# Kernel tuning notes

Measured on AMD Instinct MI355X. Metric: run time of the kernel, lower is better.

## Reference

```python
import jax, jax.numpy as jnp
import numpy as np
import math

N_HEAD = 16

def setup_inputs() -> dict:
    key = jax.random.key(0)
    k1, k2, k3, k4, k5 = jax.random.split(key, 5)
    B, S, D = 2, 2048, 1024
    return {
        "hidden_states": jax.random.normal(k1, (B, S, D), dtype=jnp.float32),
        "c_attn_w": jax.random.normal(k2, (D, 3 * D), dtype=jnp.float32) * 0.02,
        "c_attn_b": jax.random.normal(k3, (3 * D,), dtype=jnp.float32) * 0.02,
        "c_proj_w": jax.random.normal(k4, (D, D), dtype=jnp.float32) * 0.02,
        "c_proj_b": jax.random.normal(k5, (D,), dtype=jnp.float32) * 0.02,
    }

def reference(hidden_states, c_attn_w, c_attn_b, c_proj_w, c_proj_b):
    B, S, D = hidden_states.shape
    H = N_HEAD
    hd = D // H
    # GPT-2 Conv1D: x @ W + b, W is [in, out]
    qkv = hidden_states @ c_attn_w + c_attn_b            # [B,S,3D]
    q, k, v = jnp.split(qkv, 3, axis=-1)                 # each [B,S,D]
    # sparsify_q/k/v_fn are identity hooks in this config
    def to_heads(x):
        return x.reshape(B, S, H, hd).transpose(0, 2, 1, 3)  # [B,H,S,hd]
    q, k, v = to_heads(q), to_heads(k), to_heads(v)
    scores = jnp.einsum("bhqd,bhkd->bhqk", q, k) / math.sqrt(hd)  # [B,H,S,S]
    causal = jnp.triu(jnp.ones((S, S), dtype=bool), k=1)
    scores = jnp.where(causal, jnp.finfo(scores.dtype).min, scores)
    attn = jax.nn.softmax(scores, axis=-1)
    out = jnp.einsum("bhqk,bhkd->bhqd", attn, v)         # [B,H,S,hd]
    out = out.transpose(0, 2, 1, 3).reshape(B, S, D)
    return out @ c_proj_w + c_proj_b
```

## Files before the change

kernel.cpp:

```cpp
#include <hip/hip_runtime.h>
#include <stdint.h>


#define B_   2
#define S_   2048
#define D_   1024
#define H_   16
#define HD_  64

typedef __bf16 bf16x8 __attribute__((ext_vector_type(8)));
typedef float  f32x4  __attribute__((ext_vector_type(4)));
typedef float  f32x16 __attribute__((ext_vector_type(16)));
typedef uint32_t u32x4 __attribute__((ext_vector_type(4)));

__device__ __forceinline__ float b2f(uint16_t u) {
    union { uint32_t i; float f; } x; x.i = ((uint32_t)u) << 16; return x.f;
}
__device__ __forceinline__ uint16_t f2b(float f) {
    uint32_t x = __builtin_bit_cast(uint32_t, f);
    x += 0x7fffu + ((x >> 16) & 1u);
    return (uint16_t)(x >> 16);
}
__device__ __forceinline__ float sq(float f) {
    return fminf(fmaxf(f, -1e4f), 1e4f);
}
__device__ __forceinline__ void async16(const void* g, void* l) {
    __builtin_amdgcn_global_load_lds(
        (const __attribute__((address_space(1))) void*)g,
        (__attribute__((address_space(3))) void*)l, 16, 0, 0);
}

__global__ __launch_bounds__(64)
void kcode(uint16_t* out, float v) { if (threadIdx.x == 0) out[0] = f2b(v); }

__device__ __forceinline__ void cvt4(const float* __restrict__ in,
                                     uint16_t* __restrict__ out, int i) {
    float4 v = *(const float4*)(in + i);
    ushort4 o;
    o.x = f2b(v.x); o.y = f2b(v.y); o.z = f2b(v.z); o.w = f2b(v.w);
    *(ushort4*)(out + i) = o;
}

__device__ __forceinline__ void trans_body(const float* __restrict__ in,
                                           uint16_t* __restrict__ out,
                                           int rows, int cols, int bxx, int byy,
                                           int tid, uint16_t (*tile)[68]) {
    const int tx = tid & 15, ty = tid >> 4;
    const int c0 = bxx * 64, r0 = byy * 64;
#pragma unroll
    for (int p = 0; p < 4; ++p) {
        int rr = ty + p * 16;
        float4 v = *(const float4*)(in + (size_t)(r0 + rr) * cols + c0 + tx * 4);
        tile[rr][tx * 4 + 0] = f2b(v.x);
        tile[rr][tx * 4 + 1] = f2b(v.y);
        tile[rr][tx * 4 + 2] = f2b(v.z);
        tile[rr][tx * 4 + 3] = f2b(v.w);
    }
    __syncthreads();
#pragma unroll
    for (int p = 0; p < 4; ++p) {
        int rr = ty + p * 16;
        ushort4 v;
        v.x = tile[tx * 4 + 0][rr];
        v.y = tile[tx * 4 + 1][rr];
        v.z = tile[tx * 4 + 2][rr];
        v.w = tile[tx * 4 + 3][rr];
        *(ushort4*)(out + (size_t)(c0 + rr) * rows + r0 + tx * 4) = v;
    }
}

__global__ __launch_bounds__(256)
void kprep(const float* __restrict__ hid, const float* __restrict__ ab,
           const float* __restrict__ pb, const float* __restrict__ wA,
           const float* __restrict__ wP, uint16_t* __restrict__ HO,
           uint16_t* __restrict__ bA, uint16_t* __restrict__ bP,
           uint16_t* __restrict__ WtA, uint16_t* __restrict__ WtP) {
    __shared__ __attribute__((aligned(16))) uint16_t tile[64][68];
    const int bx = (int)blockIdx.x, tid = threadIdx.x;
    if (bx < 4096) {
        cvt4(hid, HO, (bx * 256 + tid) * 4);
    } else if (bx < 4100) {
        int i = ((bx - 4096) * 256 + tid) * 4;
        const float* src = (i < 3072) ? ab + i : pb + (i - 3072);
        uint16_t*   dst = (i < 3072) ? bA + i : bP + (i - 3072);
        float4 v = *(const float4*)src;
        ushort4 o;
        o.x = f2b(v.x); o.y = f2b(v.y); o.z = f2b(v.z); o.w = f2b(v.w);
        *(ushort4*)dst = o;
    } else if (bx < 4868) {
        int bb = bx - 4100;
        trans_body(wA, WtA, 1024, 3072, bb % 48, bb / 48, tid, tile);
    } else {
        int bb = bx - 4868;
        trans_body(wP, WtP, 1024, 1024, bb % 16, bb / 16, tid, tile);
    }
}

__global__ __launch_bounds__(256, 2)
void kgemm_qkv(const uint16_t* __restrict__ A, const uint16_t* __restrict__ Bt,
               const uint16_t* __restrict__ bias,
               uint16_t* __restrict__ Qb, uint16_t* __restrict__ Kb,
               uint16_t* __restrict__ Vt) {
    constexpr int KD = 1024;
    __shared__ __attribute__((aligned(16))) uint16_t smem[2][8192];
    const int tid = threadIdx.x, lane = tid & 63, wid = tid >> 6;
    const int r = lane & 15, qd = lane >> 4;
    const int bm = blockIdx.x * 128, bn = blockIdx.y * 128;
    const int wm = (wid & 1) * 64, wn = (wid >> 1) * 64;
    const int sel = (int)blockIdx.y >> 3;
    f32x4 acc[4][4] = {};

    auto stage = [&](int k0, int buf) {
        uint16_t* As = smem[buf];
        uint16_t* Bs = smem[buf] + 4096;
#pragma unroll
        for (int half = 0; half < 2; ++half) {
            int s = half * 256 + tid;
            int row = s >> 2;
            int kq = (s & 3) ^ (row & 3);
            async16(A  + (size_t)(bm + row) * KD + k0 + kq * 8, As + s * 8);
            async16(Bt + (size_t)(bn + row) * KD + k0 + kq * 8, Bs + s * 8);
        }
    };

    stage(0, 0);

    if (sel != 2) {
        for (int t = 0; t < 32; ++t) {
            __syncthreads();
            if (t + 1 < 32) stage((t + 1) * 32, (t + 1) & 1);
            const uint16_t* As = smem[t & 1];
            const uint16_t* Bs = smem[t & 1] + 4096;
            bf16x8 af[4], bfr[4];
#pragma unroll
            for (int i = 0; i < 4; ++i) {
                int ra = wm + i * 16 + r;
                af[i]  = *(const bf16x8*)(As + ((ra * 4) + (qd ^ (ra & 3))) * 8);
                int rb = wn + i * 16 + r;
                bfr[i] = *(const bf16x8*)(Bs + ((rb * 4) + (qd ^ (rb & 3))) * 8);
            }
#pragma unroll
            for (int i = 0; i < 4; ++i)
#pragma unroll
                for (int j = 0; j < 4; ++j)
                    acc[i][j] = __builtin_amdgcn_mfma_f32_16x16x32_bf16(
                        bfr[j], af[i], acc[i][j], 0, 0, 0);
        }
        const float SCq = 0.1803368801111204f;
        uint16_t* dst = sel ? Kb : Qb;
#pragma unroll
        for (int j = 0; j < 4; ++j) {
            int n0 = bn + wn + j * 16 + qd * 4;
            ushort4 b4 = *(const ushort4*)(bias + n0);
            float bv0 = b2f(b4.x), bv1 = b2f(b4.y),
                  bv2 = b2f(b4.z), bv3 = b2f(b4.w);
            int d = n0 & 1023, h = d >> 6, e0 = d & 63;
#pragma unroll
            for (int i = 0; i < 4; ++i) {
                int m = bm + wm + i * 16 + r;
                int bb = m >> 11, s = m & 2047;
                float v0 = acc[i][j][0] + bv0, v1 = acc[i][j][1] + bv1,
                      v2 = acc[i][j][2] + bv2, v3 = acc[i][j][3] + bv3;
                if (sel == 0) { v0 *= SCq; v1 *= SCq; v2 *= SCq; v3 *= SCq; }
                ushort4 o;
                o.x = f2b(sq(v0)); o.y = f2b(sq(v1));
                o.z = f2b(sq(v2)); o.w = f2b(sq(v3));
                *(ushort4*)(dst + (((size_t)bb * H_ + h) * S_ + s) * HD_ + e0) = o;
            }
        }
    } else {
        for (int t = 0; t < 32; ++t) {
            __syncthreads();
            if (t + 1 < 32) stage((t + 1) * 32, (t + 1) & 1);
            const uint16_t* As = smem[t & 1];
            const uint16_t* Bs = smem[t & 1] + 4096;
            bf16x8 af[4], bfr[4];
#pragma unroll
            for (int i = 0; i < 4; ++i) {
                int ra = wm + i * 16 + r;
                af[i]  = *(const bf16x8*)(As + ((ra * 4) + (qd ^ (ra & 3))) * 8);
                int rb = wn + i * 16 + r;
                bfr[i] = *(const bf16x8*)(Bs + ((rb * 4) + (qd ^ (rb & 3))) * 8);
            }
#pragma unroll
            for (int i = 0; i < 4; ++i)
#pragma unroll
                for (int j = 0; j < 4; ++j)
                    acc[i][j] = __builtin_amdgcn_mfma_f32_16x16x32_bf16(
                        af[i], bfr[j], acc[i][j], 0, 0, 0);
        }
#pragma unroll
        for (int j = 0; j < 4; ++j) {
            int n = bn + wn + j * 16 + r;
            float bv = b2f(bias[n]);
            int d = n & 1023, h = d >> 6, e = d & 63;
#pragma unroll
            for (int i = 0; i < 4; ++i) {
                int m0 = bm + wm + i * 16 + qd * 4;
                int bb = m0 >> 11, s0 = m0 & 2047;
                ushort4 o;
                o.x = f2b(sq(acc[i][j][0] + bv));
                o.y = f2b(sq(acc[i][j][1] + bv));
                o.z = f2b(sq(acc[i][j][2] + bv));
                o.w = f2b(sq(acc[i][j][3] + bv));
                *(ushort4*)(Vt + (((size_t)bb * H_ + h) * HD_ + e) * S_ + s0) = o;
            }
        }
    }
}

__global__ __launch_bounds__(256, 2)
void kgemm_proj(const uint16_t* __restrict__ A, const uint16_t* __restrict__ Bt,
                const uint16_t* __restrict__ bias, float* __restrict__ out) {
    constexpr int KD = 1024;
    __shared__ __attribute__((aligned(16))) uint16_t smem[2][6144];
    const int tid = threadIdx.x, lane = tid & 63, wid = tid >> 6;
    const int r = lane & 15, qd = lane >> 4;
    const int bm = blockIdx.x * 64, bn = blockIdx.y * 128;
    const int wm = (wid & 1) * 32, wn = (wid >> 1) * 64;
    f32x4 acc[2][4] = {};

    auto stage = [&](int k0, int buf) {
        uint16_t* As = smem[buf];
        uint16_t* Bs = smem[buf] + 2048;
        {
            int s = tid;
            int row = s >> 2;
            int kq = (s & 3) ^ (row & 3);
            async16(A + (size_t)(bm + row) * KD + k0 + kq * 8, As + s * 8);
        }
#pragma unroll
        for (int half = 0; half < 2; ++half) {
            int s = half * 256 + tid;
            int row = s >> 2;
            int kq = (s & 3) ^ (row & 3);
            async16(Bt + (size_t)(bn + row) * KD + k0 + kq * 8, Bs + s * 8);
        }
    };

    stage(0, 0);

    for (int t = 0; t < 32; ++t) {
        __syncthreads();
        if (t + 1 < 32) stage((t + 1) * 32, (t + 1) & 1);
        const uint16_t* As = smem[t & 1];
        const uint16_t* Bs = smem[t & 1] + 2048;
        bf16x8 af[2], bfr[4];
#pragma unroll
        for (int i = 0; i < 2; ++i) {
            int ra = wm + i * 16 + r;
            af[i] = *(const bf16x8*)(As + ((ra * 4) + (qd ^ (ra & 3))) * 8);
        }
#pragma unroll
        for (int j = 0; j < 4; ++j) {
            int rb = wn + j * 16 + r;
            bfr[j] = *(const bf16x8*)(Bs + ((rb * 4) + (qd ^ (rb & 3))) * 8);
        }
#pragma unroll
        for (int i = 0; i < 2; ++i)
#pragma unroll
            for (int j = 0; j < 4; ++j)
                acc[i][j] = __builtin_amdgcn_mfma_f32_16x16x32_bf16(
                    bfr[j], af[i], acc[i][j], 0, 0, 0);
    }

#pragma unroll
    for (int i = 0; i < 2; ++i) {
        int m = bm + wm + i * 16 + r;
#pragma unroll
        for (int j = 0; j < 4; ++j) {
            int n0 = bn + wn + j * 16 + qd * 4;
            ushort4 b4 = *(const ushort4*)(bias + n0);
            float4 o;
            o.x = sq(acc[i][j][0] + b2f(b4.x));
            o.y = sq(acc[i][j][1] + b2f(b4.y));
            o.z = sq(acc[i][j][2] + b2f(b4.z));
            o.w = sq(acc[i][j][3] + b2f(b4.w));
            *(float4*)(out + (size_t)m * 1024 + n0) = o;
        }
    }
}

__global__ __launch_bounds__(256, 4)
void kattn(const uint16_t* __restrict__ Q, const uint16_t* __restrict__ K,
           const uint16_t* __restrict__ Vt, uint16_t* __restrict__ O) {
    const int d_  = (int)blockIdx.y * 32 + (int)blockIdx.x;
    const int bh  = (d_ & 7) + 8 * ((d_ >> 3) & 3);
    const int qt  = 31 - (d_ >> 5);
    const int tid = threadIdx.x, lane = tid & 63, wid = tid >> 6;
    const int c = lane & 31, hh = lane >> 5;
    const int wq = wid >> 1, wk = wid & 1;
    const uint16_t* Qb = Q  + (size_t)bh * S_ * HD_;
    const int b = bh >> 4, h = bh & 15;

    __shared__ __attribute__((aligned(16))) uint16_t smem[4][4096];
    __shared__ float lsx[4][64];

    const int T = qt + 1;

    const int sA = tid, sB = 256 + tid;
    const int krA = sA >> 3, kcA = (sA & 7) ^ (krA & 7);
    const int krB = sB >> 3, kcB = (sB & 7) ^ (krB & 7);
    const uint16_t* ksA = K  + (size_t)bh * S_ * HD_ + (size_t)krA * HD_ + kcA * 8;
    const uint16_t* ksB = K  + (size_t)bh * S_ * HD_ + (size_t)krB * HD_ + kcB * 8;
    const uint16_t* vsA = Vt + (size_t)bh * HD_ * S_ + (size_t)krA * S_ + kcA * 8;
    const uint16_t* vsB = Vt + (size_t)bh * HD_ * S_ + (size_t)krB * S_ + kcB * 8;

    auto stageto = [&](int buf) {
        async16(ksA, &smem[buf][sA * 8]);
        async16(ksB, &smem[buf][sB * 8]);
        async16(vsA, &smem[2 + buf][sA * 8]);
        async16(vsB, &smem[2 + buf][sB * 8]);
        ksA += 64 * HD_; ksB += 64 * HD_;
        vsA += 64;       vsB += 64;
    };

    stageto(0);

    const int q0 = qt * 64;
    const int qg = q0 + wq * 32 + c;
    bf16x8 qf[4];
#pragma unroll
    for (int cc = 0; cc < 4; ++cc)
        qf[cc] = *(const bf16x8*)(Qb + (size_t)qg * HD_ + cc * 16 + hh * 8);

    const int krow = wk * 32 + c;
    const int kofs0 = krow * 64 + (((0 + hh) ^ (krow & 7)) * 8);
    const int kofs1 = krow * 64 + (((2 + hh) ^ (krow & 7)) * 8);
    const int kofs2 = krow * 64 + (((4 + hh) ^ (krow & 7)) * 8);
    const int kofs3 = krow * 64 + (((6 + hh) ^ (krow & 7)) * 8);
    const int vgA = ((4 * wk + 0 + hh) ^ (c & 7)) * 8;
    const int vgB = ((4 * wk + 2 + hh) ^ (c & 7)) * 8;
    const int vofs00 = c * 64 + vgA,        vofs01 = c * 64 + vgB;
    const int vofs10 = (32 + c) * 64 + vgA, vofs11 = (32 + c) * 64 + vgB;

    const f32x16 ZERO = {};
    f32x16 oacc0 = {}, oacc1 = {};
    float lsum = 0.f;

    auto iter = [&](int buf, int t, bool pf) {
        __syncthreads();
        if (pf) stageto(buf ^ 1);

        const uint16_t* Kc = smem[buf];
        const uint16_t* Vc = smem[2 + buf];

        __builtin_amdgcn_s_setprio(1);
        bf16x8 kf0 = *(const bf16x8*)(Kc + kofs0);
        bf16x8 kf1 = *(const bf16x8*)(Kc + kofs1);
        bf16x8 kf2 = *(const bf16x8*)(Kc + kofs2);
        bf16x8 kf3 = *(const bf16x8*)(Kc + kofs3);
        f32x16 sacc;
        sacc = __builtin_amdgcn_mfma_f32_32x32x16_bf16(kf0, qf[0], ZERO, 0, 0, 0);
        sacc = __builtin_amdgcn_mfma_f32_32x32x16_bf16(kf1, qf[1], sacc, 0, 0, 0);
        sacc = __builtin_amdgcn_mfma_f32_32x32x16_bf16(kf2, qf[2], sacc, 0, 0, 0);
        sacc = __builtin_amdgcn_mfma_f32_32x32x16_bf16(kf3, qf[3], sacc, 0, 0, 0);
        __builtin_amdgcn_s_setprio(0);

        if (t == T - 1) {
            const int kvb = t * 64 + wk * 32 + 4 * hh;
#pragma unroll
            for (int r = 0; r < 16; ++r) {
                int kvgl = kvb + (r & 3) + 8 * (r >> 2);
                if (kvgl > qg) sacc[r] = -3e38f;
            }
        }

        float p[16];
#pragma unroll
        for (int r = 0; r < 16; ++r)
            p[r] = exp2f(fminf(sacc[r], 20.f));
#pragma unroll
        for (int r = 0; r < 16; r += 4)
            lsum += ((p[r] + p[r + 1]) + (p[r + 2] + p[r + 3]));

        uint32_t D[8];
#pragma unroll
        for (int m = 0; m < 8; ++m)
            asm("v_cvt_pk_bf16_f32 %0, %1, %2"
                : "=v"(D[m]) : "v"(p[2 * m]), "v"(p[2 * m + 1]));
        asm("v_permlane32_swap_b32 %0, %1" : "+v"(D[0]), "+v"(D[2]));
        asm("v_permlane32_swap_b32 %0, %1" : "+v"(D[1]), "+v"(D[3]));
        asm("v_permlane32_swap_b32 %0, %1" : "+v"(D[4]), "+v"(D[6]));
        asm("v_permlane32_swap_b32 %0, %1" : "+v"(D[5]), "+v"(D[7]));
        u32x4 w0, w1;
        w0[0] = D[0]; w0[1] = D[1]; w0[2] = D[2]; w0[3] = D[3];
        w1[0] = D[4]; w1[1] = D[5]; w1[2] = D[6]; w1[3] = D[7];
        bf16x8 pf0 = __builtin_bit_cast(bf16x8, w0);
        bf16x8 pf1 = __builtin_bit_cast(bf16x8, w1);

        __builtin_amdgcn_s_setprio(1);
        bf16x8 v00 = *(const bf16x8*)(Vc + vofs00);
        bf16x8 v10 = *(const bf16x8*)(Vc + vofs01);
        bf16x8 v01 = *(const bf16x8*)(Vc + vofs10);
        bf16x8 v11 = *(const bf16x8*)(Vc + vofs11);
        oacc0 = __builtin_amdgcn_mfma_f32_32x32x16_bf16(pf0, v00, oacc0, 0, 0, 0);
        oacc0 = __builtin_amdgcn_mfma_f32_32x32x16_bf16(pf1, v10, oacc0, 0, 0, 0);
        oacc1 = __builtin_amdgcn_mfma_f32_32x32x16_bf16(pf0, v01, oacc1, 0, 0, 0);
        oacc1 = __builtin_amdgcn_mfma_f32_32x32x16_bf16(pf1, v11, oacc1, 0, 0, 0);
        __builtin_amdgcn_s_setprio(0);
    };

    int t = 0;
    while (t + 2 <= T) {
        iter(0, t, true);
        iter(1, t + 1, t + 2 < T);
        t += 2;
    }
    if (t < T) iter(0, t, false);

    lsum += __shfl_xor(lsum, 32);
    __syncthreads();
    float* xch = (float*)&smem[0][0];
    float* myA = xch + wid * 2048;
#pragma unroll
    for (int s = 0; s < 4; ++s) {
        f32x4 a0, a1;
#pragma unroll
        for (int g = 0; g < 4; ++g) { a0[g] = oacc0[4 * s + g]; a1[g] = oacc1[4 * s + g]; }
        *(f32x4*)(myA + 0 * 1024 + s * 256 + lane * 4) = a0;
        *(f32x4*)(myA + 1 * 1024 + s * 256 + lane * 4) = a1;
    }
    lsx[wid][lane] = lsum;
    __syncthreads();
    const int pwid = wid ^ 1;
    float lfull = lsum + lsx[pwid][lane];
    float osum[16];
#pragma unroll
    for (int s = 0; s < 4; ++s) {
        f32x4 po = *(const f32x4*)(xch + pwid * 2048 + wk * 1024 + s * 256 + lane * 4);
#pragma unroll
        for (int g = 0; g < 4; ++g)
            osum[4 * s + g] = (wk ? oacc1[4 * s + g] : oacc0[4 * s + g]) + po[g];
    }
#pragma unroll
    for (int r = 0; r < 16; ++r) {
        int qp = (r & 3) + 8 * (r >> 2) + 4 * hh;
        float inv = 1.0f / __shfl(lfull, qp);
        int qglob = q0 + wq * 32 + qp;
        int hd = wk * 32 + c;
        O[((size_t)b * S_ + qglob) * D_ + h * HD_ + hd] = f2b(sq(osum[r] * inv));
    }
}

extern "C" void kernel_launch(void* const* d_in, const int* in_sizes, int n_in,
                              void* d_out, int out_size, void* d_ws, size_t ws_size,
                              hipStream_t stream) {
    uint16_t* ws = (uint16_t*)d_ws;

    const int exp_sizes[5] = {4194304, 3145728, 3072, 1048576, 1024};
    if (n_in != 5) { kcode<<<1, 64, 0, stream>>>((uint16_t*)d_out, 2950.f); return; }
    for (int i = 0; i < 5; ++i)
        if (in_sizes[i] != exp_sizes[i]) {
            kcode<<<1, 64, 0, stream>>>((uint16_t*)d_out, 3000.f + 100.f * i); return;
        }
    if (out_size != 4194304) { kcode<<<1, 64, 0, stream>>>((uint16_t*)d_out, 2900.f); return; }

    uint16_t* WtA = ws;
    uint16_t* WtP = WtA + 3145728;
    uint16_t* bA  = WtP + 1048576;
    uint16_t* bP  = bA  + 4096;
    uint16_t* Qb  = bP  + 4096;
    uint16_t* Kb  = Qb  + 4194304;
    uint16_t* Vt  = Kb  + 4194304;
    uint16_t* HO  = Vt  + 4194304;
    const size_t NEED = (size_t)((HO + 4194304) - ws) * 2 + 16;
    if (ws_size < NEED) {
        kcode<<<1, 64, 0, stream>>>((uint16_t*)d_out, 1000.f + (float)(ws_size >> 20));
        return;
    }

    kprep<<<5124, 256, 0, stream>>>((const float*)d_in[0], (const float*)d_in[2],
                                    (const float*)d_in[4], (const float*)d_in[1],
                                    (const float*)d_in[3], HO, bA, bP, WtA, WtP);

    kgemm_qkv<<<dim3(32, 24), 256, 0, stream>>>(HO, WtA, bA, Qb, Kb, Vt);
    kattn<<<dim3(32, 32), 256, 0, stream>>>(Qb, Kb, Vt, HO);
    kgemm_proj<<<dim3(64, 8), 256, 0, stream>>>(HO, WtP, bP, (float*)d_out);
}
```

Before: 174.9 us.

## Double GEMM K-step per stage and triple-buffer attention with 128-row query tiles

Both GEMM kernels now stage 64 K-columns per barrier instead of 32. This halves the number of syncthreads and doubles the shared-memory buffers. The attention kernel moves to 512-thread blocks covering 128 query rows, with a three-deep K/V ring buffer that uses explicit vmcnt waits instead of full syncthreads. The output reduction is split into two passes to fit the smaller exchange buffer. These changes aim to cut barrier overhead and improve load/compute overlap, at the cost of more LDS per block, which may lower occupancy, and more complex causal-tail handling.

After: 325.7 us. +86.2%, slower.

```diff
diff --git a/kernel.cpp b/kernel.cpp
--- a/kernel.cpp
+++ b/kernel.cpp
@@ -102,7 +102,7 @@
                uint16_t* __restrict__ Qb, uint16_t* __restrict__ Kb,
                uint16_t* __restrict__ Vt) {
     constexpr int KD = 1024;
-    __shared__ __attribute__((aligned(16))) uint16_t smem[2][8192];
+    __shared__ __attribute__((aligned(16))) uint16_t smem[2][16384];
     const int tid = threadIdx.x, lane = tid & 63, wid = tid >> 6;
     const int r = lane & 15, qd = lane >> 4;
     const int bm = blockIdx.x * 128, bn = blockIdx.y * 128;
@@ -112,39 +112,46 @@
 
     auto stage = [&](int k0, int buf) {
         uint16_t* As = smem[buf];
-        uint16_t* Bs = smem[buf] + 4096;
-#pragma unroll
-        for (int half = 0; half < 2; ++half) {
-            int s = half * 256 + tid;
-            int row = s >> 2;
-            int kq = (s & 3) ^ (row & 3);
-            async16(A  + (size_t)(bm + row) * KD + k0 + kq * 8, As + s * 8);
-            async16(Bt + (size_t)(bn + row) * KD + k0 + kq * 8, Bs + s * 8);
-        }
+        uint16_t* Bs = smem[buf] + 8192;
+#pragma unroll
+        for (int hh = 0; hh < 2; ++hh)
+#pragma unroll
+            for (int half = 0; half < 2; ++half) {
+                int s = half * 256 + tid;
+                int row = s >> 2;
+                int kq = (s & 3) ^ (row & 3);
+                async16(A  + (size_t)(bm + row) * KD + k0 + hh * 32 + kq * 8,
+                        As + hh * 4096 + s * 8);
+                async16(Bt + (size_t)(bn + row) * KD + k0 + hh * 32 + kq * 8,
+                        Bs + hh * 4096 + s * 8);
+            }
     };
 
     stage(0, 0);
 
     if (sel != 2) {
-        for (int t = 0; t < 32; ++t) {
+        for (int t = 0; t < 16; ++t) {
             __syncthreads();
-            if (t + 1 < 32) stage((t + 1) * 32, (t + 1) & 1);
-            const uint16_t* As = smem[t & 1];
-            const uint16_t* Bs = smem[t & 1] + 4096;
-            bf16x8 af[4], bfr[4];
-#pragma unroll
-            for (int i = 0; i < 4; ++i) {
-                int ra = wm + i * 16 + r;
-                af[i]  = *(const bf16x8*)(As + ((ra * 4) + (qd ^ (ra & 3))) * 8);
-                int rb = wn + i * 16 + r;
-                bfr[i] = *(const bf16x8*)(Bs + ((rb * 4) + (qd ^ (rb & 3))) * 8);
-            }
-#pragma unroll
-            for (int i = 0; i < 4; ++i)
-#pragma unroll
-                for (int j = 0; j < 4; ++j)
-                    acc[i][j] = __builtin_amdgcn_mfma_f32_16x16x32_bf16(
-                        bfr[j], af[i], acc[i][j], 0, 0, 0);
+            if (t + 1 < 16) stage((t + 1) * 64, (t + 1) & 1);
+#pragma unroll
+            for (int hh = 0; hh < 2; ++hh) {
+                const uint16_t* As = smem[t & 1] + hh * 4096;
+                const uint16_t* Bs = smem[t & 1] + 8192 + hh * 4096;
+                bf16x8 af[4], bfr[4];
+#pragma unroll
+                for (int i = 0; i < 4; ++i) {
+                    int ra = wm + i * 16 + r;
+                    af[i]  = *(const bf16x8*)(As + ((ra * 4) + (qd ^ (ra & 3))) * 8);
+                    int rb = wn + i * 16 + r;
+                    bfr[i] = *(const bf16x8*)(Bs + ((rb * 4) + (qd ^ (rb & 3))) * 8);
+                }
+#pragma unroll
+                for (int i = 0; i < 4; ++i)
+#pragma unroll
+                    for (int j = 0; j < 4; ++j)
+                        acc[i][j] = __builtin_amdgcn_mfma_f32_16x16x32_bf16(
+                            bfr[j], af[i], acc[i][j], 0, 0, 0);
+            }
         }
         const float SCq = 0.1803368801111204f;
         uint16_t* dst = sel ? Kb : Qb;
@@ -169,25 +176,28 @@
             }
         }
     } else {
-        for (int t = 0; t < 32; ++t) {
+        for (int t = 0; t < 16; ++t) {
             __syncthreads();
-            if (t + 1 < 32) stage((t + 1) * 32, (t + 1) & 1);
-            const uint16_t* As = smem[t & 1];
-            const uint16_t* Bs = smem[t & 1] + 4096;
-            bf16x8 af[4], bfr[4];
-#pragma unroll
-            for (int i = 0; i < 4; ++i) {
-                int ra = wm + i * 16 + r;
-                af[i]  = *(const bf16x8*)(As + ((ra * 4) + (qd ^ (ra & 3))) * 8);
-                int rb = wn + i * 16 + r;
-                bfr[i] = *(const bf16x8*)(Bs + ((rb * 4) + (qd ^ (rb & 3))) * 8);
-            }
-#pragma unroll
-            for (int i = 0; i < 4; ++i)
-#pragma unroll
-                for (int j = 0; j < 4; ++j)
-                    acc[i][j] = __builtin_amdgcn_mfma_f32_16x16x32_bf16(
-                        af[i], bfr[j], acc[i][j], 0, 0, 0);
+            if (t + 1 < 16) stage((t + 1) * 64, (t + 1) & 1);
+#pragma unroll
+            for (int hh = 0; hh < 2; ++hh) {
+                const uint16_t* As = smem[t & 1] + hh * 4096;
+                const uint16_t* Bs = smem[t & 1] + 8192 + hh * 4096;
+                bf16x8 af[4], bfr[4];
+#pragma unroll
+                for (int i = 0; i < 4; ++i) {
+                    int ra = wm + i * 16 + r;
+                    af[i]  = *(const bf16x8*)(As + ((ra * 4) + (qd ^ (ra & 3))) * 8);
+                    int rb = wn + i * 16 + r;
+                    bfr[i] = *(const bf16x8*)(Bs + ((rb * 4) + (qd ^ (rb & 3))) * 8);
+                }
+#pragma unroll
+                for (int i = 0; i < 4; ++i)
+#pragma unroll
+                    for (int j = 0; j < 4; ++j)
+                        acc[i][j] = __builtin_amdgcn_mfma_f32_16x16x32_bf16(
+                            af[i], bfr[j], acc[i][j], 0, 0, 0);
+            }
         }
 #pragma unroll
         for (int j = 0; j < 4; ++j) {
@@ -213,7 +223,7 @@
 void kgemm_proj(const uint16_t* __restrict__ A, const uint16_t* __restrict__ Bt,
                 const uint16_t* __restrict__ bias, float* __restrict__ out) {
     constexpr int KD = 1024;
-    __shared__ __attribute__((aligned(16))) uint16_t smem[2][6144];
+    __shared__ __attribute__((aligned(16))) uint16_t smem[2][12288];
     const int tid = threadIdx.x, lane = tid & 63, wid = tid >> 6;
     const int r = lane & 15, qd = lane >> 4;
     const int bm = blockIdx.x * 64, bn = blockIdx.y * 128;
@@ -222,46 +232,54 @@
 
     auto stage = [&](int k0, int buf) {
         uint16_t* As = smem[buf];
-        uint16_t* Bs = smem[buf] + 2048;
-        {
-            int s = tid;
-            int row = s >> 2;
-            int kq = (s & 3) ^ (row & 3);
-            async16(A + (size_t)(bm + row) * KD + k0 + kq * 8, As + s * 8);
-        }
-#pragma unroll
-        for (int half = 0; half < 2; ++half) {
-            int s = half * 256 + tid;
-            int row = s >> 2;
-            int kq = (s & 3) ^ (row & 3);
-            async16(Bt + (size_t)(bn + row) * KD + k0 + kq * 8, Bs + s * 8);
+        uint16_t* Bs = smem[buf] + 4096;
+#pragma unroll
+        for (int hh = 0; hh < 2; ++hh) {
+            {
+                int s = tid;
+                int row = s >> 2;
+                int kq = (s & 3) ^ (row & 3);
+                async16(A + (size_t)(bm + row) * KD + k0 + hh * 32 + kq * 8,
+                        As + hh * 2048 + s * 8);
+            }
+#pragma unroll
+            for (int half = 0; half < 2; ++half) {
+                int s = half * 256 + tid;
+                int row = s >> 2;
+                int kq = (s & 3) ^ (row & 3);
+                async16(Bt + (size_t)(bn + row) * KD + k0 + hh * 32 + kq * 8,
+                        Bs + hh * 4096 + s * 8);
+            }
         }
     };
 
     stage(0, 0);
 
-    for (int t = 0; t < 32; ++t) {
+    for (int t = 0; t < 16; ++t) {
         __syncthreads();
-        if (t + 1 < 32) stage((t + 1) * 32, (t + 1) & 1);
-        const uint16_t* As = smem[t & 1];
-        const uint16_t* Bs = smem[t & 1] + 2048;
-        bf16x8 af[2], bfr[4];
-#pragma unroll
-        for (int i = 0; i < 2; ++i) {
-            int ra = wm + i * 16 + r;
-            af[i] = *(const bf16x8*)(As + ((ra * 4) + (qd ^ (ra & 3))) * 8);
-        }
-#pragma unroll
-        for (int j = 0; j < 4; ++j) {
-            int rb = wn + j * 16 + r;
-            bfr[j] = *(const bf16x8*)(Bs + ((rb * 4) + (qd ^ (rb & 3))) * 8);
-        }
-#pragma unroll
-        for (int i = 0; i < 2; ++i)
-#pragma unroll
-            for (int j = 0; j < 4; ++j)
-                acc[i][j] = __builtin_amdgcn_mfma_f32_16x16x32_bf16(
-                    bfr[j], af[i], acc[i][j], 0, 0, 0);
+        if (t + 1 < 16) stage((t + 1) * 64, (t + 1) & 1);
+#pragma unroll
+        for (int hh = 0; hh < 2; ++hh) {
+            const uint16_t* As = smem[t & 1] + hh * 2048;
+            const uint16_t* Bs = smem[t & 1] + 4096 + hh * 4096;
+            bf16x8 af[2], bfr[4];
+#pragma unroll
+            for (int i = 0; i < 2; ++i) {
+                int ra = wm + i * 16 + r;
+                af[i] = *(const bf16x8*)(As + ((ra * 4) + (qd ^ (ra & 3))) * 8);
+            }
+#pragma unroll
+            for (int j = 0; j < 4; ++j) {
+                int rb = wn + j * 16 + r;
+                bfr[j] = *(const bf16x8*)(Bs + ((rb * 4) + (qd ^ (rb & 3))) * 8);
+            }
+#pragma unroll
+            for (int i = 0; i < 2; ++i)
+#pragma unroll
+                for (int j = 0; j < 4; ++j)
+                    acc[i][j] = __builtin_amdgcn_mfma_f32_16x16x32_bf16(
+                        bfr[j], af[i], acc[i][j], 0, 0, 0);
+        }
     }
 
 #pragma unroll
@@ -281,43 +299,38 @@
     }
 }
 
-__global__ __launch_bounds__(256, 4)
+__global__ __launch_bounds__(512, 6)
 void kattn(const uint16_t* __restrict__ Q, const uint16_t* __restrict__ K,
            const uint16_t* __restrict__ Vt, uint16_t* __restrict__ O) {
     const int d_  = (int)blockIdx.y * 32 + (int)blockIdx.x;
     const int bh  = (d_ & 7) + 8 * ((d_ >> 3) & 3);
-    const int qt  = 31 - (d_ >> 5);
+    const int qt  = 15 - (d_ >> 5);
     const int tid = threadIdx.x, lane = tid & 63, wid = tid >> 6;
     const int c = lane & 31, hh = lane >> 5;
     const int wq = wid >> 1, wk = wid & 1;
-    const uint16_t* Qb = Q  + (size_t)bh * S_ * HD_;
+    const uint16_t* Qb = Q + (size_t)bh * S_ * HD_;
     const int b = bh >> 4, h = bh & 15;
 
-    __shared__ __attribute__((aligned(16))) uint16_t smem[4][4096];
-    __shared__ float lsx[4][64];
-
-    const int T = qt + 1;
-
-    const int sA = tid, sB = 256 + tid;
-    const int krA = sA >> 3, kcA = (sA & 7) ^ (krA & 7);
-    const int krB = sB >> 3, kcB = (sB & 7) ^ (krB & 7);
-    const uint16_t* ksA = K  + (size_t)bh * S_ * HD_ + (size_t)krA * HD_ + kcA * 8;
-    const uint16_t* ksB = K  + (size_t)bh * S_ * HD_ + (size_t)krB * HD_ + kcB * 8;
-    const uint16_t* vsA = Vt + (size_t)bh * HD_ * S_ + (size_t)krA * S_ + kcA * 8;
-    const uint16_t* vsB = Vt + (size_t)bh * HD_ * S_ + (size_t)krB * S_ + kcB * 8;
+    __shared__ __attribute__((aligned(16))) uint16_t sbuf[6][4096];
+    __shared__ float lsx[8][64];
+
+    const int T = 2 * (qt + 1);
+
+    const int sr = tid >> 3, sc = (tid & 7) ^ (sr & 7);
+    const uint16_t* ksA = K  + (size_t)bh * S_ * HD_ + (size_t)sr * HD_ + sc * 8;
+    const uint16_t* vsA = Vt + (size_t)bh * HD_ * S_ + (size_t)sr * S_ + sc * 8;
 
     auto stageto = [&](int buf) {
-        async16(ksA, &smem[buf][sA * 8]);
-        async16(ksB, &smem[buf][sB * 8]);
-        async16(vsA, &smem[2 + buf][sA * 8]);
-        async16(vsB, &smem[2 + buf][sB * 8]);
-        ksA += 64 * HD_; ksB += 64 * HD_;
-        vsA += 64;       vsB += 64;
+        async16(ksA, &sbuf[buf][(size_t)tid * 8]);
+        async16(vsA, &sbuf[3 + buf][(size_t)tid * 8]);
+        ksA += 64 * HD_;
+        vsA += 64;
     };
 
     stageto(0);
-
-    const int q0 = qt * 64;
+    stageto(1);
+
+    const int q0 = qt * 128;
     const int qg = q0 + wq * 32 + c;
     bf16x8 qf[4];
 #pragma unroll
@@ -332,18 +345,22 @@
     const int vgA = ((4 * wk + 0 + hh) ^ (c & 7)) * 8;
     const int vgB = ((4 * wk + 2 + hh) ^ (c & 7)) * 8;
     const int vofs00 = c * 64 + vgA,        vofs01 = c * 64 + vgB;
-    const int vofs10 = (32 + c) * 64 + vgA, vofs11 = (32 + c) * 64 + vgB;
+    const int vofs10 = (32 + c) * 64 + (((4 * wk + 0 + hh) ^ ((32 + c) & 7)) * 8);
+    const int vofs11 = (32 + c) * 64 + (((4 * wk + 2 + hh) ^ ((32 + c) & 7)) * 8);
 
     const f32x16 ZERO = {};
     f32x16 oacc0 = {}, oacc1 = {};
     float lsum = 0.f;
 
-    auto iter = [&](int buf, int t, bool pf) {
-        __syncthreads();
-        if (pf) stageto(buf ^ 1);
-
-        const uint16_t* Kc = smem[buf];
-        const uint16_t* Vc = smem[2 + buf];
+    auto iterK = [&](int buf, int sb, int t, bool last, bool pf) {
+        if (last) asm volatile("s_waitcnt vmcnt(0)" ::: "memory");
+        else      asm volatile("s_waitcnt vmcnt(2)" ::: "memory");
+        __builtin_amdgcn_s_barrier();
+        asm volatile("" ::: "memory");
+        if (pf) stageto(sb);
+
+        const uint16_t* Kc = sbuf[buf];
+        const uint16_t* Vc = sbuf[3 + buf];
 
         __builtin_amdgcn_s_setprio(1);
         bf16x8 kf0 = *(const bf16x8*)(Kc + kofs0);
@@ -357,7 +374,7 @@
         sacc = __builtin_amdgcn_mfma_f32_32x32x16_bf16(kf3, qf[3], sacc, 0, 0, 0);
         __builtin_amdgcn_s_setprio(0);
 
-        if (t == T - 1) {
+        if (t >= T - 2) {
             const int kvb = t * 64 + wk * 32 + 4 * hh;
 #pragma unroll
             for (int r = 0; r < 16; ++r) {
@@ -402,44 +419,62 @@
     };
 
     int t = 0;
-    while (t + 2 <= T) {
-        iter(0, t, true);
-        iter(1, t + 1, t + 2 < T);
-        t += 2;
-    }
-    if (t < T) iter(0, t, false);
+    while (t + 3 < T) {
+        iterK(0, 2, t,     false, true);
+        iterK(1, 0, t + 1, false, true);
+        iterK(2, 1, t + 2, false, (t + 4 < T));
+        t += 3;
+    }
+    {
+        int r = T - t;
+        if (r == 3) {
+            iterK(0, 2, t,     false, true);
+            iterK(1, 0, t + 1, false, false);
+            iterK(2, 1, t + 2, true,  false);
+        } else if (r == 2) {
+            iterK(0, 2, t,     false, false);
+            iterK(1, 0, t + 1, true,  false);
+        } else {
+            iterK(0, 2, t, true, false);
+        }
+    }
 
     lsum += __shfl_xor(lsum, 32);
-    __syncthreads();
-    float* xch = (float*)&smem[0][0];
-    float* myA = xch + wid * 2048;
-#pragma unroll
-    for (int s = 0; s < 4; ++s) {
-        f32x4 a0, a1;
-#pragma unroll
-        for (int g = 0; g < 4; ++g) { a0[g] = oacc0[4 * s + g]; a1[g] = oacc1[4 * s + g]; }
-        *(f32x4*)(myA + 0 * 1024 + s * 256 + lane * 4) = a0;
-        *(f32x4*)(myA + 1 * 1024 + s * 256 + lane * 4) = a1;
-    }
     lsx[wid][lane] = lsum;
-    __syncthreads();
-    const int pwid = wid ^ 1;
-    float lfull = lsum + lsx[pwid][lane];
-    float osum[16];
-#pragma unroll
-    for (int s = 0; s < 4; ++s) {
-        f32x4 po = *(const f32x4*)(xch + pwid * 2048 + wk * 1024 + s * 256 + lane * 4);
-#pragma unroll
-        for (int g = 0; g < 4; ++g)
-            osum[4 * s + g] = (wk ? oacc1[4 * s + g] : oacc0[4 * s + g]) + po[g];
-    }
-#pragma unroll
-    for (int r = 0; r < 16; ++r) {
-        int qp = (r & 3) + 8 * (r >> 2) + 4 * hh;
-        float inv = 1.0f / __shfl(lfull, qp);
-        int qglob = q0 + wq * 32 + qp;
-        int hd = wk * 32 + c;
-        O[((size_t)b * S_ + qglob) * D_ + h * HD_ + hd] = f2b(sq(osum[r] * inv));
+    float* xch = (float*)&sbuf[0][0];
+#pragma unroll
+    for (int hp = 0; hp < 2; ++hp) {
+        __syncthreads();
+        float* myA = xch + wid * 1024;
+#pragma unroll
+        for (int s = 0; s < 4; ++s) {
+            f32x4 a;
+#pragma unroll
+            for (int g = 0; g < 4; ++g)
+                a[g] = hp ? oacc1[4 * s + g] : oacc0[4 * s + g];
+            *(f32x4*)(myA + s * 256 + lane * 4) = a;
+        }
+        __syncthreads();
+        if (wk == hp) {
+            float lfull = lsum + lsx[wid ^ 1][lane];
+            const float* pA = xch + (wid ^ 1) * 1024;
+#pragma unroll
+            for (int s = 0; s < 4; ++s) {
+                f32x4 po = *(const f32x4*)(pA + s * 256 + lane * 4);
+#pragma unroll
+                for (int g = 0; g < 4; ++g) {
+                    int r = 4 * s + g;
+                    float own = hp ? oacc1[r] : oacc0[r];
+                    float osv = own + po[g];
+                    int qp = (r & 3) + 8 * (r >> 2) + 4 * hh;
+                    float inv = 1.0f / __shfl(lfull, qp);
+                    int qglob = q0 + wq * 32 + qp;
+                    int hd = hp * 32 + c;
+                    O[((size_t)b * S_ + qglob) * D_ + h * HD_ + hd] =
+                        f2b(sq(osv * inv));
+                }
+            }
+        }
     }
 }
 
@@ -475,6 +510,6 @@
                                     (const float*)d_in[3], HO, bA, bP, WtA, WtP);
 
     kgemm_qkv<<<dim3(32, 24), 256, 0, stream>>>(HO, WtA, bA, Qb, Kb, Vt);
-    kattn<<<dim3(32, 32), 256, 0, stream>>>(Qb, Kb, Vt, HO);
+    kattn<<<dim3(32, 16), 512, 0, stream>>>(Qb, Kb, Vt, HO);
     kgemm_proj<<<dim3(64, 8), 256, 0, stream>>>(HO, WtP, bP, (float*)d_out);
 }
```
